# Optimization experiments

Measured on AMD Instinct MI355X. Metric: run time of the kernel, lower is better.

Reference implementation:

```python
import jax, jax.numpy as jnp
import numpy as np

NF, IN_NF, N_LAYERS = 64, 196, 3
B, H, W = 1, 256, 256
P3 = [(1, 1), (1, 1)]
P1 = [(0, 0), (0, 0)]


def conv2d(x, w, pad):
    return jax.lax.conv_general_dilated(x, w, (1, 1), pad,
                                        dimension_numbers=('NCHW', 'OIHW', 'NCHW'))


def prelu(x, a):
    return jnp.where(x >= 0, x, a[None, :, None, None] * x)


def warp(x, flow):
    # standard backward bilinear warp, zero padding outside the image
    Bx, C, Hx, Wx = x.shape
    yy, xx = jnp.meshgrid(jnp.arange(Hx, dtype=x.dtype),
                          jnp.arange(Wx, dtype=x.dtype), indexing='ij')
    px = xx[None] + flow[:, 0]  # (B,H,W)
    py = yy[None] + flow[:, 1]

    def sample(img, px, py):  # img (C,H,W); px,py (H,W)
        x0 = jnp.floor(px)
        y0 = jnp.floor(py)
        x1 = x0 + 1.0
        y1 = y0 + 1.0
        wx1 = px - x0
        wx0 = 1.0 - wx1
        wy1 = py - y0
        wy0 = 1.0 - wy1

        def gather(xi, yi):
            valid = (xi >= 0) & (xi <= Wx - 1) & (yi >= 0) & (yi <= Hx - 1)
            xc = jnp.clip(xi, 0, Wx - 1).astype(jnp.int32)
            yc = jnp.clip(yi, 0, Hx - 1).astype(jnp.int32)
            return img[:, yc, xc] * valid.astype(img.dtype)

        return (gather(x0, y0) * (wx0 * wy0) + gather(x1, y0) * (wx1 * wy0)
                + gather(x0, y1) * (wx0 * wy1) + gather(x1, y1) * (wx1 * wy1))

    return jax.vmap(sample)(x, px, py)


def setup_inputs() -> dict:
    key = jax.random.key(0)
    ks = jax.random.split(key, 11)
    s = 0.05
    return {
        'feat_0': jax.random.normal(ks[0], (B, 64, H, W), jnp.float32),
        'feat_1': jax.random.normal(ks[1], (B, 64, H, W), jnp.float32),
        'feat_dense': jax.random.normal(ks[2], (B, 64, H, W), jnp.float32),
        'flow': jax.random.normal(ks[3], (B, 4, H, W), jnp.float32),
        'space_mask': jax.random.uniform(ks[4], (B, 1, H, W), jnp.float32),
        'head_w': jax.random.normal(ks[5], (IN_NF, IN_NF, 3, 3), jnp.float32) * s,
        'head_a': jnp.full((IN_NF,), 0.25, jnp.float32),
        'conv_w': jax.random.normal(ks[6], (N_LAYERS, IN_NF, IN_NF, 3, 3), jnp.float32) * s,
        'conv_a': jnp.full((N_LAYERS, IN_NF), 0.25, jnp.float32),
        'last_w': jax.random.normal(ks[7], (4 + NF, IN_NF * (N_LAYERS + 1), 1, 1), jnp.float32) * s,
        'last_b': jax.random.normal(ks[8], (4 + NF,), jnp.float32) * s,
        'mask_w': jax.random.normal(ks[9], (2, NF, 3, 3), jnp.float32) * s,
        'mask_b': jax.random.normal(ks[10], (2,), jnp.float32) * s,
    }


def reference(feat_0, feat_1, feat_dense, flow, space_mask,
              head_w, head_a, conv_w, conv_a, last_w, last_b, mask_w, mask_b):
    f0 = warp(feat_0, flow[:, :2])
    f1 = warp(feat_1, flow[:, 2:4])
    x = jnp.concatenate([f0, f1, feat_dense, flow], axis=1)  # (B, in_nf, H, W)
    sm_up = jnp.repeat(jnp.repeat(space_mask, 2, axis=2), 2, axis=3)

    # head: conv3x3 -> PReLU, then mask (dense / use_sparsity=False path)
    x = prelu(conv2d(x, head_w, P3), head_a) * space_mask
    outs = [x]
    for i in range(N_LAYERS):
        x = conv2d(x, conv_w[i], P3) * space_mask
        x = prelu(x, conv_a[i])
        outs.append(x)
    x = conv2d(jnp.concatenate(outs, axis=1), last_w, P1) + last_b[None, :, None, None]

    smn = conv2d(x[:, 4:], mask_w, P3) + mask_b[None, :, None, None]

    Bx, Cx, Hx, Wx = x.shape
    x_up = jax.image.resize(x, (Bx, Cx, 2 * Hx, 2 * Wx), method='bilinear')
    smn_up = jax.image.resize(smn, (Bx, 2, 2 * Hx, 2 * Wx), method='bilinear')

    flow_out = x_up[:, :4]
    feat_t = x_up[:, 4:]
    # eval-mode mask (training=False): hard argmax between channel 0 and 1
    mask_next = (smn_up[:, :1] > smn_up[:, 1:2]).astype(x.dtype) * sm_up
    return flow_out, feat_t, mask_next
```

## Files before the change

### kernel.cpp

```cpp
#include <hip/hip_runtime.h>

typedef _Float16 f16;
typedef _Float16 f16x8 __attribute__((ext_vector_type(8)));
typedef _Float16 f16x4 __attribute__((ext_vector_type(4)));
typedef float    f32x4 __attribute__((ext_vector_type(4)));
typedef float    f32x16 __attribute__((ext_vector_type(16)));

#define MFMA16(a,b,c) __builtin_amdgcn_mfma_f32_16x16x32_f16(a,b,c,0,0,0)
#define MFMA32(a,b,c) __builtin_amdgcn_mfma_f32_32x32x16_f16(a,b,c,0,0,0)

#define NPIX 65536
#define PXS   8
#define KHS   2064
#define K16S  4128
#define HS    8256
#define CBS   16512
#define ROWH  115584
#define RBYTES 231168
#define SBUF  ((size_t)258*RBYTES)

#define PKSTEP 7168
#define PK_CONV 903168

#define PKL_CB  5120
#define PKL_BI  35840

__global__ void k_pack_conv(const float* __restrict__ head_w,
                            const float* __restrict__ conv_w,
                            f16* __restrict__ dst)
{
    int t = blockIdx.x*256 + threadIdx.x;
    int lane = t & 63; t >>= 6;
    int ob  = t % 7;  t /= 7;
    int sel = t & 1;  t >>= 1;
    int kx  = t % 3;  t /= 3;
    int k16 = t & 1;  t >>= 1;
    int cb  = t % 7;  t /= 7;
    int ky  = t % 3;  t /= 3;
    int li  = t;
    if (li >= 4) return;
    const float* W = (li == 0) ? head_w : (conv_w + (size_t)(li-1)*196*196*9);
    int oc  = ob*32 + (lane & 31);
    int ic0 = cb*32 + k16*16 + (lane >> 5)*8;
    int tap = ky*3 + kx;
    f16x8 v;
#pragma unroll
    for (int j = 0; j < 8; ++j) {
        int ic = ic0 + j;
        float x = 0.f;
        if (oc < 196 && ic < 196) x = W[((size_t)oc*196 + ic)*9 + tap];
        f16 h = (f16)x;
        v[j] = (sel == 0) ? h : (f16)(x - (float)h);
    }
    size_t frag = (((((size_t)(ky*7+cb)*2 + k16)*3 + kx)*2 + sel)*7 + ob);
    *(f16x8*)(dst + (size_t)li*PK_CONV + frag*512 + (size_t)lane*8) = v;
}

__global__ void k_pack_last(const float* __restrict__ last_w, f16* __restrict__ dst)
{
    int t = blockIdx.x*256 + threadIdx.x;
    if (t >= 4*7*5*2*64) return;
    int lane = t & 63; t >>= 6;
    int sel  = t & 1;  t >>= 1;
    int ob   = t % 5;  t /= 5;
    int cb   = t % 7;  t /= 7;
    int bi   = t;
    int oc = ob*16 + (lane & 15);
    int k0 = cb*32 + (lane >> 4)*8;
    f16x8 v;
#pragma unroll
    for (int j = 0; j < 8; ++j) {
        int k = k0 + j;
        float x = 0.f;
        if (oc < 68 && k < 196) x = last_w[(size_t)oc*784 + bi*196 + k];
        f16 h = (f16)x;
        v[j] = (sel == 0) ? h : (f16)(x - (float)h);
    }
    *(f16x8*)(dst + (((size_t)((bi*7+cb)*5 + ob)*2 + sel)*64 + lane)*8) = v;
}

__global__ void k_zero_halo(f16* __restrict__ bufA, f16* __restrict__ bufB)
{
    int c = blockIdx.x*256 + threadIdx.x;
    int end = c & 1; c >>= 1;
    int kh  = c & 1; c >>= 1;
    int k16 = c & 1; c >>= 1;
    int h   = c & 1; c >>= 1;
    int cb  = c % 7; c /= 7;
    int row = c % 258; c /= 258;
    if (c >= 2) return;
    f16* base = (c == 0) ? bufA : bufB;
    f16* p = base + (size_t)row*ROWH + cb*CBS + h*HS + k16*K16S + kh*KHS + (end ? 257 : 0)*PXS;
    f16x8 z = {(f16)0,(f16)0,(f16)0,(f16)0,(f16)0,(f16)0,(f16)0,(f16)0};
    *(f16x8*)p = z;
}

struct Gath { int o00,o01,o10,o11; float w00,w01,w10,w11; };

__device__ inline Gath mk_gath(float pxf, float pyf)
{
    float x0 = floorf(pxf), y0 = floorf(pyf);
    float x1 = x0 + 1.f, y1 = y0 + 1.f;
    float wx1 = pxf - x0, wx0 = 1.f - wx1;
    float wy1 = pyf - y0, wy0 = 1.f - wy1;
    bool vx0 = (x0 >= 0.f) && (x0 <= 255.f);
    bool vx1 = (x1 >= 0.f) && (x1 <= 255.f);
    bool vy0 = (y0 >= 0.f) && (y0 <= 255.f);
    bool vy1 = (y1 >= 0.f) && (y1 <= 255.f);
    int ix0 = min(max((int)x0, 0), 255);
    int ix1 = min(max((int)x1, 0), 255);
    int iy0 = min(max((int)y0, 0), 255);
    int iy1 = min(max((int)y1, 0), 255);
    Gath g;
    g.o00 = iy0*256 + ix0; g.w00 = (vx0 && vy0) ? wx0*wy0 : 0.f;
    g.o01 = iy0*256 + ix1; g.w01 = (vx1 && vy0) ? wx1*wy0 : 0.f;
    g.o10 = iy1*256 + ix0; g.w10 = (vx0 && vy1) ? wx0*wy1 : 0.f;
    g.o11 = iy1*256 + ix1; g.w11 = (vx1 && vy1) ? wx1*wy1 : 0.f;
    return g;
}

__device__ inline void store4n(f16* __restrict__ rowb, int slot, int c0,
                               float a, float b, float c, float d)
{
    f16x4 hi, lo;
    f16 h;
    h = (f16)a; hi[0] = h; lo[0] = (f16)(a - (float)h);
    h = (f16)b; hi[1] = h; lo[1] = (f16)(b - (float)h);
    h = (f16)c; hi[2] = h; lo[2] = (f16)(c - (float)h);
    h = (f16)d; hi[3] = h; lo[3] = (f16)(d - (float)h);
    int cb = c0 >> 5, w32 = c0 & 31;
    f16* p = rowb + cb*CBS + (w32 >> 4)*K16S + ((w32 >> 3) & 1)*KHS
                 + (size_t)slot*PXS + (w32 & 7);
    *(f16x4*)p        = hi;
    *(f16x4*)(p + HS) = lo;
}

__global__ void k_warp_concat(const float* __restrict__ f0, const float* __restrict__ f1,
                              const float* __restrict__ fd, const float* __restrict__ flow,
                              f16* __restrict__ out)
{
    int px = blockIdx.x*256 + threadIdx.x;
    int row = px >> 8, col = px & 255;
    f16* rowb = out + (size_t)(row+1)*ROWH;
    int slot = col + 1;
    Gath g0 = mk_gath((float)col + flow[px],          (float)row + flow[NPIX   + px]);
    Gath g1 = mk_gath((float)col + flow[2*NPIX + px], (float)row + flow[3*NPIX + px]);
#pragma unroll
    for (int c = 0; c < 64; c += 4) {
        float v[4];
#pragma unroll
        for (int r = 0; r < 4; ++r) {
            const float* im = f0 + (size_t)(c+r)*NPIX;
            v[r] = g0.w00*im[g0.o00] + g0.w01*im[g0.o01] + g0.w10*im[g0.o10] + g0.w11*im[g0.o11];
        }
        store4n(rowb, slot, c, v[0], v[1], v[2], v[3]);
    }
#pragma unroll
    for (int c = 0; c < 64; c += 4) {
        float v[4];
#pragma unroll
        for (int r = 0; r < 4; ++r) {
            const float* im = f1 + (size_t)(c+r)*NPIX;
            v[r] = g1.w00*im[g1.o00] + g1.w01*im[g1.o01] + g1.w10*im[g1.o10] + g1.w11*im[g1.o11];
        }
        store4n(rowb, slot, 64 + c, v[0], v[1], v[2], v[3]);
    }
#pragma unroll
    for (int c = 0; c < 64; c += 4) {
        store4n(rowb, slot, 128 + c, fd[(size_t)(c+0)*NPIX + px], fd[(size_t)(c+1)*NPIX + px],
                                     fd[(size_t)(c+2)*NPIX + px], fd[(size_t)(c+3)*NPIX + px]);
    }
    store4n(rowb, slot, 192, flow[px], flow[NPIX+px], flow[2*NPIX+px], flow[3*NPIX+px]);
#pragma unroll
    for (int c = 196; c < 224; c += 4) store4n(rowb, slot, c, 0.f, 0.f, 0.f, 0.f);
}

template<int NOB, int OB0>
__device__ __forceinline__ void mfma_step(const char* bb, const f16x8* Bh, const f16x8* Bl,
                                          f32x16 (&acc)[4][2], int lane)
{
#pragma unroll
    for (int o = 0; o < NOB; ++o) {
        f16x8 Ah = *(const f16x8*)(bb + (OB0 + o)*1024 + lane*16);
        f16x8 Al = *(const f16x8*)(bb + (7 + OB0 + o)*1024 + lane*16);
#pragma unroll
        for (int pt = 0; pt < 2; ++pt) {
            acc[o][pt] = MFMA32(Ah, Bh[pt], acc[o][pt]);
            acc[o][pt] = MFMA32(Al, Bh[pt], acc[o][pt]);
            acc[o][pt] = MFMA32(Ah, Bl[pt], acc[o][pt]);
        }
    }
}

__global__ __launch_bounds__(256, 2)
void k_conv32(const f16* __restrict__ in, f16* __restrict__ out,
              const f16* __restrict__ pack, const float* __restrict__ alpha,
              const float* __restrict__ mask)
{
    __shared__ __align__(16) char As[2][14336];

    int bid = blockIdx.x;
    int wg  = (bid & 7)*64 + (bid >> 3);
    int row  = wg >> 1;
    int half = wg & 1;
    int tid  = threadIdx.x;
    int lane = tid & 63;
    int w    = tid >> 6;
    int ocg  = w >> 1;
    int pxg  = w & 1;
    int l31 = lane & 31, lk = lane >> 5;
    int colbase = half*128 + pxg*64;

    f32x16 acc[4][2];
#pragma unroll
    for (int o = 0; o < 4; ++o)
#pragma unroll
        for (int pt = 0; pt < 2; ++pt)
#pragma unroll
            for (int e = 0; e < 16; ++e) acc[o][pt][e] = 0.f;

    auto stage = [&](int b, const f16* src) {
        __builtin_amdgcn_global_load_lds(
            (const __attribute__((address_space(1))) void*)(src + (size_t)tid*8),
            (__attribute__((address_space(3))) void*)(&As[b][0] + tid*16), 16, 0, 0);
        __builtin_amdgcn_global_load_lds(
            (const __attribute__((address_space(1))) void*)(src + (size_t)(tid+256)*8),
            (__attribute__((address_space(3))) void*)(&As[b][0] + (tid+256)*16), 16, 0, 0);
        __builtin_amdgcn_global_load_lds(
            (const __attribute__((address_space(1))) void*)(src + (size_t)(tid+512)*8),
            (__attribute__((address_space(3))) void*)(&As[b][0] + (tid+512)*16), 16, 0, 0);
        if (tid < 128)
            __builtin_amdgcn_global_load_lds(
                (const __attribute__((address_space(1))) void*)(src + (size_t)(tid+768)*8),
                (__attribute__((address_space(3))) void*)(&As[b][0] + (tid+768)*16), 16, 0, 0);
    };

    auto lB = [&](const f16* bp, f16x8* H, f16x8* L) {
        H[0] = *(const f16x8*)bp;
        L[0] = *(const f16x8*)(bp + HS);
        H[1] = *(const f16x8*)(bp + 32*PXS);
        L[1] = *(const f16x8*)(bp + 32*PXS + HS);
    };

    const f16* bwave = in + (size_t)row*ROWH + (size_t)lk*KHS + (size_t)(colbase + l31)*PXS;

    f16x8 Bh0[2], Bl0[2], Bh1[2], Bl1[2];
    stage(0, pack);
    lB(bwave, Bh0, Bl0);
    __syncthreads();

    int bsel = 0;
    int q = 0;
    for (int ky = 0; ky < 3; ++ky) {
        const f16* brow = bwave + (size_t)ky*ROWH;
        for (int cb = 0; cb < 7; ++cb) {
            const f16* bcb = brow + cb*CBS;
            const f16* bnext = (cb < 6) ? (bcb + CBS) : (brow + ROWH);
#pragma unroll
            for (int k16 = 0; k16 < 2; ++k16) {
#pragma unroll
                for (int kx = 0; kx < 3; ++kx) {
                    bool lastPhase = (ky == 2) && (cb == 6) && (k16 == 1) && (kx == 2);
                    if (!lastPhase) {
                        stage(bsel ^ 1, pack + (size_t)(q+1)*PKSTEP);
                        const f16* nb;
                        if (kx < 2)        nb = bcb + k16*K16S + (kx+1)*PXS;
                        else if (k16 == 0) nb = bcb + K16S;
                        else               nb = bnext;
                        lB(nb, Bh1, Bl1);
                    }
                    const char* bb = &As[bsel][0];
                    if (ocg == 0) mfma_step<4,0>(bb, Bh0, Bl0, acc, lane);
                    else          mfma_step<3,4>(bb, Bh0, Bl0, acc, lane);
                    __syncthreads();
                    bsel ^= 1; ++q;
                    Bh0[0] = Bh1[0]; Bh0[1] = Bh1[1];
                    Bl0[0] = Bl1[0]; Bl0[1] = Bl1[1];
                }
            }
        }
    }

    int nob = (ocg == 0) ? 4 : 3;
    int ob0 = (ocg == 0) ? 0 : 4;
    float mv[2];
#pragma unroll
    for (int pt = 0; pt < 2; ++pt) mv[pt] = mask[row*256 + colbase + pt*32 + l31];
#pragma unroll
    for (int o = 0; o < 4; ++o) {
        if (o >= nob) continue;
        int ob = ob0 + o;
#pragma unroll
        for (int qg = 0; qg < 4; ++qg) {
            int oc0 = ob*32 + 8*qg + 4*lk;
            f32x4 a4 = *(const f32x4*)(alpha + min(oc0, 192));
#pragma unroll
            for (int pt = 0; pt < 2; ++pt) {
                f16x4 hi, lo;
#pragma unroll
                for (int e = 0; e < 4; ++e) {
                    float v = acc[o][pt][qg*4 + e];
                    v = (v >= 0.f ? v : a4[e]*v) * mv[pt];
                    f16 h = (f16)v;
                    hi[e] = h;
                    lo[e] = (f16)(v - (float)h);
                }
                f16* p = out + (size_t)(row+1)*ROWH + (size_t)(colbase + pt*32 + l31 + 1)*PXS
                       + lk*4 + ob*CBS + (qg >> 1)*K16S + (qg & 1)*KHS;
                *(f16x4*)p        = hi;
                *(f16x4*)(p + HS) = lo;
            }
        }
    }
}

__global__ __launch_bounds__(256, 4)
void k_acc_last(const f16* __restrict__ in, const f16* __restrict__ pack,
                const float* __restrict__ bias, float* __restrict__ accp, int bi)
{
    int lane = threadIdx.x & 63;
    int wid  = (blockIdx.x << 2) | (threadIdx.x >> 6);
    int row  = wid >> 3;
    int col0 = (wid & 7) << 5;
    int l15 = lane & 15, lk = lane >> 4;

    f32x4 acc[5][2];
#pragma unroll
    for (int i = 0; i < 5; ++i)
#pragma unroll
        for (int j = 0; j < 2; ++j)
            acc[i][j] = (f32x4){0.f, 0.f, 0.f, 0.f};

    const f16* bb = in + (size_t)(row+1)*ROWH + (size_t)(col0 + l15 + 1)*PXS
                  + (lk >> 1)*K16S + (lk & 1)*KHS;
    const f16* ap = pack + (size_t)bi*PKL_BI + (size_t)lane*8;
    for (int cb = 0; cb < 7; ++cb) {
        f16x8 bh[2], bl[2];
#pragma unroll
        for (int pb = 0; pb < 2; ++pb) {
            const f16* p = bb + cb*CBS + pb*16*PXS;
            bh[pb] = *(const f16x8*)p;
            bl[pb] = *(const f16x8*)(p + HS);
        }
        const f16* a = ap + cb*PKL_CB;
#pragma unroll
        for (int ob = 0; ob < 5; ++ob) {
            f16x8 ah = *(const f16x8*)(a + ob*1024);
            f16x8 al = *(const f16x8*)(a + ob*1024 + 512);
#pragma unroll
            for (int pb = 0; pb < 2; ++pb) {
                acc[ob][pb] = MFMA16(ah, bh[pb], acc[ob][pb]);
                acc[ob][pb] = MFMA16(ah, bl[pb], acc[ob][pb]);
                acc[ob][pb] = MFMA16(al, bh[pb], acc[ob][pb]);
            }
        }
    }
#pragma unroll
    for (int ob = 0; ob < 5; ++ob) {
        int oc0 = ob*16 + lk*4;
        if (oc0 >= 72) continue;
#pragma unroll
        for (int pb = 0; pb < 2; ++pb) {
            int px = row*256 + col0 + pb*16 + l15;
            float* dst = accp + (size_t)px*72 + oc0;
            f32x4 d = acc[ob][pb];
            if (bi == 0) {
                f32x4 b4;
#pragma unroll
                for (int r = 0; r < 4; ++r) b4[r] = bias[min(oc0 + r, 67)];
                *(f32x4*)dst = d + b4;
            } else {
                *(f32x4*)dst = *(const f32x4*)dst + d;
            }
        }
    }
}

__global__ void k_smn(const float* __restrict__ accp, const float* __restrict__ mw,
                      const float* __restrict__ mb, float* __restrict__ smn)
{
    int px = blockIdx.x*256 + threadIdx.x;
    int row = px >> 8, col = px & 255;
    float s0 = mb[0], s1 = mb[1];
    for (int ky = 0; ky < 3; ++ky) {
        int r = row + ky - 1;
        if ((unsigned)r > 255u) continue;
        for (int kx = 0; kx < 3; ++kx) {
            int c = col + kx - 1;
            if ((unsigned)c > 255u) continue;
            const float* ab = accp + ((size_t)r*256 + c)*72 + 4;
            const float* w  = mw + ky*3 + kx;
#pragma unroll
            for (int ch = 0; ch < 64; ch += 4) {
                f32x4 v = *(const f32x4*)(ab + ch);
                s0 += v[0]*w[(ch+0)*9] + v[1]*w[(ch+1)*9] + v[2]*w[(ch+2)*9] + v[3]*w[(ch+3)*9];
                s1 += v[0]*w[(64+ch+0)*9] + v[1]*w[(64+ch+1)*9] + v[2]*w[(64+ch+2)*9] + v[3]*w[(64+ch+3)*9];
            }
        }
    }
    smn[px]        = s0;
    smn[NPIX + px] = s1;
}

__global__ void k_upsample(const float* __restrict__ accp, float* __restrict__ outp)
{
    int o = blockIdx.x*256 + threadIdx.x;
    int oy = o >> 9, ox = o & 511;
    int my = oy >> 1, mx = ox >> 1;
    int r0, r1, c0, c1; float wy0, wy1, wx0, wx1;
    if (oy & 1) { r0 = my;            r1 = min(my+1, 255); wy0 = 0.75f; wy1 = 0.25f; }
    else        { r0 = max(my-1, 0);  r1 = my;             wy0 = 0.25f; wy1 = 0.75f; }
    if (ox & 1) { c0 = mx;            c1 = min(mx+1, 255); wx0 = 0.75f; wx1 = 0.25f; }
    else        { c0 = max(mx-1, 0);  c1 = mx;             wx0 = 0.25f; wx1 = 0.75f; }
    const float* p00 = accp + ((size_t)r0*256 + c0)*72;
    const float* p01 = accp + ((size_t)r0*256 + c1)*72;
    const float* p10 = accp + ((size_t)r1*256 + c0)*72;
    const float* p11 = accp + ((size_t)r1*256 + c1)*72;
    float w00 = wy0*wx0, w01 = wy0*wx1, w10 = wy1*wx0, w11 = wy1*wx1;
#pragma unroll
    for (int ch = 0; ch < 68; ch += 4) {
        f32x4 va = *(const f32x4*)(p00 + ch);
        f32x4 vb = *(const f32x4*)(p01 + ch);
        f32x4 vc = *(const f32x4*)(p10 + ch);
        f32x4 vd = *(const f32x4*)(p11 + ch);
        f32x4 v;
#pragma unroll
        for (int r = 0; r < 4; ++r)
            v[r] = w00*va[r] + w01*vb[r] + w10*vc[r] + w11*vd[r];
        outp[(size_t)(ch+0)*262144 + o] = v[0];
        outp[(size_t)(ch+1)*262144 + o] = v[1];
        outp[(size_t)(ch+2)*262144 + o] = v[2];
        outp[(size_t)(ch+3)*262144 + o] = v[3];
    }
}

__global__ void k_mask(const float* __restrict__ smn, const float* __restrict__ sm,
                       float* __restrict__ outp)
{
    int o = blockIdx.x*256 + threadIdx.x;
    int oy = o >> 9, ox = o & 511;
    int my = oy >> 1, mx = ox >> 1;
    int r0, r1, c0, c1; float wy0, wy1, wx0, wx1;
    if (oy & 1) { r0 = my;            r1 = min(my+1, 255); wy0 = 0.75f; wy1 = 0.25f; }
    else        { r0 = max(my-1, 0);  r1 = my;             wy0 = 0.25f; wy1 = 0.75f; }
    if (ox & 1) { c0 = mx;            c1 = min(mx+1, 255); wx0 = 0.75f; wx1 = 0.25f; }
    else        { c0 = max(mx-1, 0);  c1 = mx;             wx0 = 0.25f; wx1 = 0.75f; }
    float w00 = wy0*wx0, w01 = wy0*wx1, w10 = wy1*wx0, w11 = wy1*wx1;
    int i00 = r0*256 + c0, i01 = r0*256 + c1, i10 = r1*256 + c0, i11 = r1*256 + c1;
    float s0 = w00*smn[i00] + w01*smn[i01] + w10*smn[i10] + w11*smn[i11];
    float s1 = w00*smn[NPIX+i00] + w01*smn[NPIX+i01] + w10*smn[NPIX+i10] + w11*smn[NPIX+i11];
    outp[(size_t)68*262144 + o] = (s0 > s1) ? sm[my*256 + mx] : 0.f;
}

extern "C" void kernel_launch(void* const* d_in, const int* in_sizes, int n_in,
                              void* d_out, int out_size, void* d_ws, size_t ws_size,
                              hipStream_t stream)
{
    const float* feat0  = (const float*)d_in[0];
    const float* feat1  = (const float*)d_in[1];
    const float* featd  = (const float*)d_in[2];
    const float* flow   = (const float*)d_in[3];
    const float* smask  = (const float*)d_in[4];
    const float* head_w = (const float*)d_in[5];
    const float* head_a = (const float*)d_in[6];
    const float* conv_w = (const float*)d_in[7];
    const float* conv_a = (const float*)d_in[8];
    const float* last_w = (const float*)d_in[9];
    const float* last_b = (const float*)d_in[10];
    const float* mask_w = (const float*)d_in[11];
    const float* mask_b = (const float*)d_in[12];
    float* outp = (float*)d_out;

    char* ws = (char*)d_ws;
    size_t off = 0;
    f16* bufA = (f16*)(ws + off); off += SBUF;
    f16* bufB = (f16*)(ws + off); off += SBUF;
    f16* packc = (f16*)(ws + off); off += (size_t)4*PK_CONV*2;
    f16* packl = (f16*)(ws + off); off += (size_t)4*PKL_BI*2;
    float* accp = (float*)(ws + off); off += (size_t)NPIX*72*4;
    float* smn  = (float*)(ws + off); off += (size_t)2*NPIX*4;

    hipMemsetAsync(bufA, 0, RBYTES, stream);
    hipMemsetAsync((char*)bufA + (size_t)257*RBYTES, 0, RBYTES, stream);
    hipMemsetAsync(bufB, 0, RBYTES, stream);
    hipMemsetAsync((char*)bufB + (size_t)257*RBYTES, 0, RBYTES, stream);
    k_zero_halo<<<226, 256, 0, stream>>>(bufA, bufB);

    k_pack_conv<<<1764, 256, 0, stream>>>(head_w, conv_w, packc);
    k_pack_last<<<70, 256, 0, stream>>>(last_w, packl);
    k_warp_concat<<<256, 256, 0, stream>>>(feat0, feat1, featd, flow, bufA);

    k_conv32<<<512, 256, 0, stream>>>(bufA, bufB, packc, head_a, smask);
    k_acc_last<<<512, 256, 0, stream>>>(bufB, packl, last_b, accp, 0);
    k_conv32<<<512, 256, 0, stream>>>(bufB, bufA, packc + (size_t)1*PK_CONV, conv_a, smask);
    k_acc_last<<<512, 256, 0, stream>>>(bufA, packl, last_b, accp, 1);
    k_conv32<<<512, 256, 0, stream>>>(bufA, bufB, packc + (size_t)2*PK_CONV, conv_a + 196, smask);
    k_acc_last<<<512, 256, 0, stream>>>(bufB, packl, last_b, accp, 2);
    k_conv32<<<512, 256, 0, stream>>>(bufB, bufA, packc + (size_t)3*PK_CONV, conv_a + 392, smask);
    k_acc_last<<<512, 256, 0, stream>>>(bufA, packl, last_b, accp, 3);

    k_smn<<<256, 256, 0, stream>>>(accp, mask_w, mask_b, smn);
    k_upsample<<<1024, 256, 0, stream>>>(accp, outp);
    k_mask<<<1024, 256, 0, stream>>>(smn, smask, outp);
}
```

Baseline: 835.1 us.

## Stage activation tiles in LDS and read conv weights directly from global

The 3x3 conv main loop swaps what it stages. It now stages the input activation row tile (130 pixels, both k-halves, hi/lo planes) into double-buffered LDS once per (ky, cb) phase and reads the packed weights straight from global memory per wave. This cuts the barrier count from 126 per block to 21 and lets the three kx shifts reuse one staged activation tile instead of reloading B fragments from global for every kx. It also alternates the out-channel group assignment per block, aiming to balance the 4-vs-3 output-block imbalance across waves. The cost is that weight loads are now uncached-in-LDS global reads, repeated by every block and served only by L2.

```diff
diff --git a/kernel.cpp b/kernel.cpp
--- a/kernel.cpp
+++ b/kernel.cpp
@@ -19,11 +19,14 @@
 #define RBYTES 231168
 #define SBUF  ((size_t)258*RBYTES)
 
-#define PKSTEP 7168
+#define PKSUB  7168
+#define PKCB   43008
 #define PK_CONV 903168
 
 #define PKL_CB  5120
 #define PKL_BI  35840
+
+#define BSTG 16640
 
 __global__ void k_pack_conv(const float* __restrict__ head_w,
                             const float* __restrict__ conv_w,
@@ -176,18 +179,27 @@
 }
 
 template<int NOB, int OB0>
-__device__ __forceinline__ void mfma_step(const char* bb, const f16x8* Bh, const f16x8* Bl,
-                                          f32x16 (&acc)[4][2], int lane)
-{
+__device__ __forceinline__ void sub_step(const f16* __restrict__ ws, const char* __restrict__ bs,
+                                         f32x16 (&acc)[4][2])
+{
+    f16x8 Ah[NOB], Al[NOB];
 #pragma unroll
     for (int o = 0; o < NOB; ++o) {
-        f16x8 Ah = *(const f16x8*)(bb + (OB0 + o)*1024 + lane*16);
-        f16x8 Al = *(const f16x8*)(bb + (7 + OB0 + o)*1024 + lane*16);
+        Ah[o] = *(const f16x8*)(ws + (OB0 + o)*512);
+        Al[o] = *(const f16x8*)(ws + 3584 + (OB0 + o)*512);
+    }
+    f16x8 Bh[2], Bl[2];
+    Bh[0] = *(const f16x8*)(bs);
+    Bl[0] = *(const f16x8*)(bs + 4*2080);
+    Bh[1] = *(const f16x8*)(bs + 512);
+    Bl[1] = *(const f16x8*)(bs + 512 + 4*2080);
+#pragma unroll
+    for (int o = 0; o < NOB; ++o) {
 #pragma unroll
         for (int pt = 0; pt < 2; ++pt) {
-            acc[o][pt] = MFMA32(Ah, Bh[pt], acc[o][pt]);
-            acc[o][pt] = MFMA32(Al, Bh[pt], acc[o][pt]);
-            acc[o][pt] = MFMA32(Ah, Bl[pt], acc[o][pt]);
+            acc[o][pt] = MFMA32(Ah[o], Bh[pt], acc[o][pt]);
+            acc[o][pt] = MFMA32(Al[o], Bh[pt], acc[o][pt]);
+            acc[o][pt] = MFMA32(Ah[o], Bl[pt], acc[o][pt]);
         }
     }
 }
@@ -197,7 +209,7 @@
               const f16* __restrict__ pack, const float* __restrict__ alpha,
               const float* __restrict__ mask)
 {
-    __shared__ __align__(16) char As[2][14336];
+    __shared__ __align__(16) char Bs[2][BSTG];
 
     int bid = blockIdx.x;
     int wg  = (bid & 7)*64 + (bid >> 3);
@@ -206,10 +218,10 @@
     int tid  = threadIdx.x;
     int lane = tid & 63;
     int w    = tid >> 6;
-    int ocg  = w >> 1;
+    int ocg  = ((w >> 1) ^ bid) & 1;
     int pxg  = w & 1;
     int l31 = lane & 31, lk = lane >> 5;
-    int colbase = half*128 + pxg*64;
+    int cb0 = half*128;
 
     f32x16 acc[4][2];
 #pragma unroll
@@ -219,70 +231,57 @@
 #pragma unroll
             for (int e = 0; e < 16; ++e) acc[o][pt][e] = 0.f;
 
-    auto stage = [&](int b, const f16* src) {
-        __builtin_amdgcn_global_load_lds(
-            (const __attribute__((address_space(1))) void*)(src + (size_t)tid*8),
-            (__attribute__((address_space(3))) void*)(&As[b][0] + tid*16), 16, 0, 0);
-        __builtin_amdgcn_global_load_lds(
-            (const __attribute__((address_space(1))) void*)(src + (size_t)(tid+256)*8),
-            (__attribute__((address_space(3))) void*)(&As[b][0] + (tid+256)*16), 16, 0, 0);
-        __builtin_amdgcn_global_load_lds(
-            (const __attribute__((address_space(1))) void*)(src + (size_t)(tid+512)*8),
-            (__attribute__((address_space(3))) void*)(&As[b][0] + (tid+512)*16), 16, 0, 0);
-        if (tid < 128)
-            __builtin_amdgcn_global_load_lds(
-                (const __attribute__((address_space(1))) void*)(src + (size_t)(tid+768)*8),
-                (__attribute__((address_space(3))) void*)(&As[b][0] + (tid+768)*16), 16, 0, 0);
+    auto stage = [&](int b, const f16* g) {
+#pragma unroll
+        for (int u = 0; u < 5; ++u) {
+            int c = tid + u*256;
+            if (u < 4 || c < 1040) {
+                int pl = c / 130;
+                int i  = c - pl*130;
+                const f16* src = g + (size_t)pl*KHS + (size_t)(cb0 + i)*PXS;
+                __builtin_amdgcn_global_load_lds(
+                    (const __attribute__((address_space(1))) void*)src,
+                    (__attribute__((address_space(3))) void*)(&Bs[b][0] + c*16),
+                    16, 0, 0);
+            }
+        }
     };
 
-    auto lB = [&](const f16* bp, f16x8* H, f16x8* L) {
-        H[0] = *(const f16x8*)bp;
-        L[0] = *(const f16x8*)(bp + HS);
-        H[1] = *(const f16x8*)(bp + 32*PXS);
-        L[1] = *(const f16x8*)(bp + 32*PXS + HS);
-    };
-
-    const f16* bwave = in + (size_t)row*ROWH + (size_t)lk*KHS + (size_t)(colbase + l31)*PXS;
-
-    f16x8 Bh0[2], Bl0[2], Bh1[2], Bl1[2];
-    stage(0, pack);
-    lB(bwave, Bh0, Bl0);
+    const int lbase = lk*2080 + (pxg*64 + l31)*16;
+
+    const f16* g = in + (size_t)row*ROWH;
+    stage(0, g);
     __syncthreads();
 
-    int bsel = 0;
-    int q = 0;
-    for (int ky = 0; ky < 3; ++ky) {
-        const f16* brow = bwave + (size_t)ky*ROWH;
-        for (int cb = 0; cb < 7; ++cb) {
-            const f16* bcb = brow + cb*CBS;
-            const f16* bnext = (cb < 6) ? (bcb + CBS) : (brow + ROWH);
-#pragma unroll
-            for (int k16 = 0; k16 < 2; ++k16) {
-#pragma unroll
-                for (int kx = 0; kx < 3; ++kx) {
-                    bool lastPhase = (ky == 2) && (cb == 6) && (k16 == 1) && (kx == 2);
-                    if (!lastPhase) {
-                        stage(bsel ^ 1, pack + (size_t)(q+1)*PKSTEP);
-                        const f16* nb;
-                        if (kx < 2)        nb = bcb + k16*K16S + (kx+1)*PXS;
-                        else if (k16 == 0) nb = bcb + K16S;
-                        else               nb = bnext;
-                        lB(nb, Bh1, Bl1);
-                    }
-                    const char* bb = &As[bsel][0];
-                    if (ocg == 0) mfma_step<4,0>(bb, Bh0, Bl0, acc, lane);
-                    else          mfma_step<3,4>(bb, Bh0, Bl0, acc, lane);
-                    __syncthreads();
-                    bsel ^= 1; ++q;
-                    Bh0[0] = Bh1[0]; Bh0[1] = Bh1[1];
-                    Bl0[0] = Bl1[0]; Bl0[1] = Bl1[1];
-                }
-            }
-        }
+    int bsel = 0, cbc = 0;
+    for (int ph = 0; ph < 21; ++ph) {
+        if (ph < 20) {
+            if (cbc < 6) { g += CBS; ++cbc; }
+            else         { g += ROWH - 6*CBS; cbc = 0; }
+            stage(bsel ^ 1, g);
+        }
+        const f16* wcb = pack + (size_t)ph*PKCB + (size_t)lane*8;
+        const char* bl = &Bs[bsel][0] + lbase;
+        if (ocg == 0) {
+#pragma unroll
+            for (int k16 = 0; k16 < 2; ++k16)
+#pragma unroll
+                for (int kx = 0; kx < 3; ++kx)
+                    sub_step<4,0>(wcb + (k16*3+kx)*PKSUB, bl + k16*4160 + kx*16, acc);
+        } else {
+#pragma unroll
+            for (int k16 = 0; k16 < 2; ++k16)
+#pragma unroll
+                for (int kx = 0; kx < 3; ++kx)
+                    sub_step<3,4>(wcb + (k16*3+kx)*PKSUB, bl + k16*4160 + kx*16, acc);
+        }
+        __syncthreads();
+        bsel ^= 1;
     }
 
     int nob = (ocg == 0) ? 4 : 3;
     int ob0 = (ocg == 0) ? 0 : 4;
+    int colbase = cb0 + pxg*64;
     float mv[2];
 #pragma unroll
     for (int pt = 0; pt < 2; ++pt) mv[pt] = mask[row*256 + colbase + pt*32 + l31];
```

Result: no change. 851.5 us (+2.0%).

## Relax conv barrier to vmcnt wait, add MFMA priority, alternate wave roles

Applied to the files above, without the earlier changes.

The full __syncthreads in the k_conv32 loop becomes an s_waitcnt vmcnt(4) plus a raw s_barrier. This waits only for the LDS-staged weight loads and leaves the next B-operand register loads in flight across the barrier. MFMA sections run under s_setprio(1), and the 4-versus-3 output-block wave split now alternates by block index to balance work across SIMDs. The weight-staging loop is made branch-free, so the upper threads issue redundant duplicate loads of the last chunk, which adds a little memory traffic.

```diff
diff --git a/kernel.cpp b/kernel.cpp
--- a/kernel.cpp
+++ b/kernel.cpp
@@ -19,7 +19,7 @@
 #define RBYTES 231168
 #define SBUF  ((size_t)258*RBYTES)
 
-#define PKSTEP 7168
+#define PKSUB  7168
 #define PK_CONV 903168
 
 #define PKL_CB  5120
@@ -206,7 +206,7 @@
     int tid  = threadIdx.x;
     int lane = tid & 63;
     int w    = tid >> 6;
-    int ocg  = w >> 1;
+    int ocg  = ((w >> 1) ^ bid) & 1;
     int pxg  = w & 1;
     int l31 = lane & 31, lk = lane >> 5;
     int colbase = half*128 + pxg*64;
@@ -220,19 +220,17 @@
             for (int e = 0; e < 16; ++e) acc[o][pt][e] = 0.f;
 
     auto stage = [&](int b, const f16* src) {
+#pragma unroll
+        for (int u = 0; u < 3; ++u) {
+            int c = tid + u*256;
+            __builtin_amdgcn_global_load_lds(
+                (const __attribute__((address_space(1))) void*)(src + (size_t)c*8),
+                (__attribute__((address_space(3))) void*)(&As[b][0] + c*16), 16, 0, 0);
+        }
+        int c4 = 768 + (tid & 127);
         __builtin_amdgcn_global_load_lds(
-            (const __attribute__((address_space(1))) void*)(src + (size_t)tid*8),
-            (__attribute__((address_space(3))) void*)(&As[b][0] + tid*16), 16, 0, 0);
-        __builtin_amdgcn_global_load_lds(
-            (const __attribute__((address_space(1))) void*)(src + (size_t)(tid+256)*8),
-            (__attribute__((address_space(3))) void*)(&As[b][0] + (tid+256)*16), 16, 0, 0);
-        __builtin_amdgcn_global_load_lds(
-            (const __attribute__((address_space(1))) void*)(src + (size_t)(tid+512)*8),
-            (__attribute__((address_space(3))) void*)(&As[b][0] + (tid+512)*16), 16, 0, 0);
-        if (tid < 128)
-            __builtin_amdgcn_global_load_lds(
-                (const __attribute__((address_space(1))) void*)(src + (size_t)(tid+768)*8),
-                (__attribute__((address_space(3))) void*)(&As[b][0] + (tid+768)*16), 16, 0, 0);
+            (const __attribute__((address_space(1))) void*)(src + (size_t)c4*8),
+            (__attribute__((address_space(3))) void*)(&As[b][0] + c4*16), 16, 0, 0);
     };
 
     auto lB = [&](const f16* bp, f16x8* H, f16x8* L) {
@@ -247,7 +245,8 @@
     f16x8 Bh0[2], Bl0[2], Bh1[2], Bl1[2];
     stage(0, pack);
     lB(bwave, Bh0, Bl0);
-    __syncthreads();
+    asm volatile("s_waitcnt vmcnt(4)" ::: "memory");
+    __builtin_amdgcn_s_barrier();
 
     int bsel = 0;
     int q = 0;
@@ -262,7 +261,7 @@
                 for (int kx = 0; kx < 3; ++kx) {
                     bool lastPhase = (ky == 2) && (cb == 6) && (k16 == 1) && (kx == 2);
                     if (!lastPhase) {
-                        stage(bsel ^ 1, pack + (size_t)(q+1)*PKSTEP);
+                        stage(bsel ^ 1, pack + (size_t)(q+1)*PKSUB);
                         const f16* nb;
                         if (kx < 2)        nb = bcb + k16*K16S + (kx+1)*PXS;
                         else if (k16 == 0) nb = bcb + K16S;
@@ -270,9 +269,14 @@
                         lB(nb, Bh1, Bl1);
                     }
                     const char* bb = &As[bsel][0];
+                    __builtin_amdgcn_s_setprio(1);
                     if (ocg == 0) mfma_step<4,0>(bb, Bh0, Bl0, acc, lane);
                     else          mfma_step<3,4>(bb, Bh0, Bl0, acc, lane);
-                    __syncthreads();
+                    __builtin_amdgcn_s_setprio(0);
+                    if (!lastPhase) {
+                        asm volatile("s_waitcnt vmcnt(4)" ::: "memory");
+                        __builtin_amdgcn_s_barrier();
+                    }
                     bsel ^= 1; ++q;
                     Bh0[0] = Bh1[0]; Bh0[1] = Bh1[1];
                     Bl0[0] = Bl1[0]; Bl0[1] = Bl1[1];
```

Measured after the change: 871.2 us. 4.3% more time.
